# Kernel tuning notes

Measured on AMD Instinct MI355X. Metric: run time of the kernel, lower is better.

## Reference

```python
import jax, jax.numpy as jnp
import numpy as np

B, Q, K, D, H = 2, 1024, 4096, 1024, 16
DH = D // H
LN_EPS = 1e-5


def setup_inputs() -> dict:
    key = jax.random.key(0)
    ks = jax.random.split(key, 10)
    queries = jax.random.normal(ks[0], (B, Q, D), jnp.float32)
    keys = jax.random.normal(ks[1], (B, K, D), jnp.float32)
    values = jax.random.normal(ks[2], (B, K, D), jnp.float32)
    # 128 words of 8 query tokens each: boundaries 0,8,...,1024 (sorted, unique)
    word_boundaries = jnp.arange(0, Q + 1, 8, dtype=jnp.int32)  # [129]
    # monotone map from query positions to char/key positions in [0, K]
    char_boundaries = jnp.sort(jax.random.randint(ks[3], (Q,), 0, K + 1, dtype=jnp.int32))
    s = 0.02
    ln_gamma = jnp.ones((D,), jnp.float32)
    ln_beta = jnp.zeros((D,), jnp.float32)
    in_proj_w = jax.random.normal(ks[4], (3 * D, D), jnp.float32) * s
    in_proj_b = jnp.zeros((3 * D,), jnp.float32)
    out_w = jax.random.normal(ks[5], (D, D), jnp.float32) * s
    out_b = jnp.zeros((D,), jnp.float32)
    return dict(queries=queries, keys=keys, values=values,
                word_boundaries=word_boundaries, char_boundaries=char_boundaries,
                ln_gamma=ln_gamma, ln_beta=ln_beta,
                in_proj_w=in_proj_w, in_proj_b=in_proj_b,
                out_w=out_w, out_b=out_b)


def char_aware_mask(wb, cb, q_len, k_len):
    """Vectorized version of the per-word python loop.
    Float mask of 0/1 (PyTorch ADDS a float attn_mask to the scores)."""
    ws, we = wb[:-1], wb[1:]                     # word start/end in query coords [nW]
    nW = ws.shape[0]
    cs = cb[ws]                                  # char span start per word
    ce = cb[we - 1]                              # char span end per word
    q = jnp.arange(q_len)
    i = jnp.clip(jnp.searchsorted(wb, q, side='right') - 1, 0, nW - 1)  # word id per query row
    valid = (q >= ws[i]) & (q < we[i])           # rows actually written by the loop
    j = jnp.arange(k_len)[None, :]               # [1, K]
    in_char = (j >= cs[i][:, None]) & (j < ce[i][:, None])
    # prev word: keys [wb[i-1], wb[i]) (query-coord indices used on key axis, as in source)
    ps = ws[jnp.maximum(i - 1, 0)]
    in_prev = (i > 0)[:, None] & (j >= ps[:, None]) & (j < ws[i][:, None])
    # next word: keys [wb[i+1], wb[i+2])
    ns = we[i]
    ne = wb[jnp.minimum(i + 2, nW)]
    in_next = (i < nW - 1)[:, None] & (j >= ns[:, None]) & (j < ne[:, None])
    return (valid[:, None] & (in_char | in_prev | in_next)).astype(jnp.float32)


def reference(queries, keys, values, word_boundaries, char_boundaries,
              ln_gamma, ln_beta, in_proj_w, in_proj_b, out_w, out_b):
    b, q_len, d = queries.shape
    k_len = keys.shape[1]
    mask = char_aware_mask(word_boundaries, char_boundaries, q_len, k_len)  # [Q, K]
    # LayerNorm(queries)
    mu = jnp.mean(queries, axis=-1, keepdims=True)
    var = jnp.var(queries, axis=-1, keepdims=True)
    x = (queries - mu) * jax.lax.rsqrt(var + LN_EPS) * ln_gamma + ln_beta
    # MultiheadAttention(x, keys, values, attn_mask=mask) -- float mask added to logits
    wq, wk, wv = jnp.split(in_proj_w, 3, axis=0)
    bq, bk, bv = jnp.split(in_proj_b, 3)
    qh = (x @ wq.T + bq).reshape(b, q_len, H, DH)
    kh = (keys @ wk.T + bk).reshape(b, k_len, H, DH)
    vh = (values @ wv.T + bv).reshape(b, k_len, H, DH)
    scale = 1.0 / jnp.sqrt(jnp.asarray(DH, queries.dtype))
    scores = jnp.einsum('bqhd,bkhd->bhqk', qh * scale, kh) + mask[None, None]
    attn = jax.nn.softmax(scores, axis=-1)
    ctx = jnp.einsum('bhqk,bkhd->bqhd', attn, vh).reshape(b, q_len, d)
    out = ctx @ out_w.T + out_b
    # residual; dropout is identity at inference
    return queries + out
```

## Files before the change

### kernel.cpp

```cpp
#include <hip/hip_runtime.h>
#include <hip/hip_bf16.h>


typedef __attribute__((ext_vector_type(8))) short bf16x8;
typedef __attribute__((ext_vector_type(4))) float f32x4;
typedef __attribute__((ext_vector_type(16))) float f32x16;

#define L2E 1.44269504088896341f
#define CSCALE (0.125f * L2E)
#define NSPLIT 4

__device__ __forceinline__ short f2bf(float f) {
  __hip_bfloat16 h = __float2bfloat16(f);
  return reinterpret_cast<short&>(h);
}

__device__ __forceinline__ unsigned cvtpk(float a, float b) {
  unsigned r;
  asm("v_cvt_pk_bf16_f32 %0, %1, %2" : "=v"(r) : "v"(a), "v"(b));
  return r;
}

__device__ __forceinline__ float fexp2(float x) {
#if __has_builtin(__builtin_amdgcn_exp2f)
  return __builtin_amdgcn_exp2f(x);
#else
  float r;
  asm("v_exp_f32 %0, %1" : "=v"(r) : "v"(x));
  return r;
#endif
}

__device__ __forceinline__ void halfswap(unsigned a, unsigned b, unsigned& x, unsigned& y) {
#if __has_builtin(__builtin_amdgcn_permlane32_swap)
  auto r = __builtin_amdgcn_permlane32_swap(a, b, false, false);
  x = (unsigned)r[0];
  y = (unsigned)r[1];
#else
  unsigned ca = (unsigned)__shfl_xor((int)a, 32);
  unsigned cb = (unsigned)__shfl_xor((int)b, 32);
  bool h = ((threadIdx.x & 63) >> 5) != 0;
  x = h ? cb : a;
  y = h ? b : ca;
#endif
}

__device__ __forceinline__ void gload16(const void* g, void* l) {
  __builtin_amdgcn_global_load_lds(
      (const __attribute__((address_space(1))) void*)g,
      (__attribute__((address_space(3))) void*)l, 16, 0, 0);
}

template <int N>
__device__ __forceinline__ void pipe_barrier() {
  __builtin_amdgcn_sched_barrier(0);
  if constexpr (N == 8)
    asm volatile("s_waitcnt vmcnt(8) lgkmcnt(0)" ::: "memory");
  else if constexpr (N == 6)
    asm volatile("s_waitcnt vmcnt(6) lgkmcnt(0)" ::: "memory");
  else if constexpr (N == 2)
    asm volatile("s_waitcnt vmcnt(2) lgkmcnt(0)" ::: "memory");
  else
    asm volatile("s_waitcnt vmcnt(0) lgkmcnt(0)" ::: "memory");
  __builtin_amdgcn_s_barrier();
  __builtin_amdgcn_sched_barrier(0);
}

__device__ __forceinline__ void lds_barrier() {
  __builtin_amdgcn_sched_barrier(0);
  __builtin_amdgcn_s_barrier();
  __builtin_amdgcn_sched_barrier(0);
}

__global__ __launch_bounds__(256) void prep_kernel(const float* __restrict__ w,
                                                   const float* __restrict__ o,
                                                   short* __restrict__ dw,
                                                   short* __restrict__ dof,
                                                   const float* __restrict__ x,
                                                   const float* __restrict__ gamma,
                                                   const float* __restrict__ beta,
                                                   short* __restrict__ xout,
                                                   const int* __restrict__ wb,
                                                   const int* __restrict__ cb,
                                                   int* __restrict__ iv,
                                                   const float* __restrict__ keys,
                                                   const float* __restrict__ values,
                                                   short* __restrict__ kbf,
                                                   short* __restrict__ vbf) {
  const int blk = blockIdx.x;
  const int t = threadIdx.x;
  if (blk < 4096) {
    long i = ((long)blk * 256 + t) * 4;
    const float* s;
    short* d;
    if (i < 3145728) { s = w + i; d = dw + i; }
    else { s = o + (i - 3145728); d = dof + (i - 3145728); }
    float4 xv = *(const float4*)s;
    uint2 r;
    r.x = cvtpk(xv.x, xv.y);
    r.y = cvtpk(xv.z, xv.w);
    *(uint2*)d = r;
  } else if (blk < 6144) {
    const int row = blk - 4096;
    float4 v = ((const float4*)(x + (size_t)row * 1024))[t];
    float s = v.x + v.y + v.z + v.w;
    float ss = v.x * v.x + v.y * v.y + v.z * v.z + v.w * v.w;
#pragma unroll
    for (int d = 32; d; d >>= 1) { s += __shfl_xor(s, d); ss += __shfl_xor(ss, d); }
    __shared__ float red[8];
    int wv2 = t >> 6, lane = t & 63;
    if (lane == 0) { red[wv2] = s; red[4 + wv2] = ss; }
    __syncthreads();
    s = red[0] + red[1] + red[2] + red[3];
    ss = red[4] + red[5] + red[6] + red[7];
    float mean = s * (1.0f / 1024.0f);
    float var = ss * (1.0f / 1024.0f) - mean * mean;
    float rstd = rsqrtf(var + 1e-5f);
    float4 g = ((const float4*)gamma)[t];
    float4 b = ((const float4*)beta)[t];
    uint2 oo;
    oo.x = cvtpk((v.x - mean) * rstd * g.x + b.x, (v.y - mean) * rstd * g.y + b.y);
    oo.y = cvtpk((v.z - mean) * rstd * g.z + b.z, (v.w - mean) * rstd * g.w + b.w);
    ((uint2*)(xout + (size_t)row * 1024))[t] = oo;
  } else if (blk < 6148) {
    int q = (blk - 6144) * 256 + t;
    if (q >= 1024) return;
    int cnt = 0;
    for (int k = 0; k < 129; ++k) cnt += (wb[k] <= q) ? 1 : 0;
    int i = cnt - 1;
    i = i < 0 ? 0 : (i > 127 ? 127 : i);
    bool valid = (q >= wb[i]) && (q < wb[i + 1]);
    int cs = 0, ce = 0, pl = 0, ph = 0, nl = 0, nh = 0;
    if (valid) {
      cs = cb[wb[i]];
      ce = cb[wb[i + 1] - 1];
      if (i > 0) { pl = wb[i - 1]; ph = wb[i]; }
      if (i < 127) { nl = wb[i + 1]; nh = wb[(i + 2 <= 128) ? i + 2 : 128]; }
    }
    int* p = iv + q * 8;
    p[0] = cs; p[1] = ce; p[2] = pl; p[3] = ph; p[4] = nl; p[5] = nh; p[6] = 0; p[7] = 0;
  } else {
    long i = ((long)(blk - 6148) * 256 + t) * 4;
    const float* s;
    short* d;
    if (i < 8388608) { s = keys + i; d = kbf + i; }
    else { s = values + (i - 8388608); d = vbf + (i - 8388608); }
    float4 xv = *(const float4*)s;
    uint2 r;
    r.x = cvtpk(xv.x, xv.y);
    r.y = cvtpk(xv.z, xv.w);
    *(uint2*)d = r;
  }
}

__device__ __forceinline__ unsigned inrange3(int key, const int* p) {
  bool m = (key >= p[0] && key < p[1]) || (key >= p[2] && key < p[3]) ||
           (key >= p[4] && key < p[5]);
  return m ? 1u : 0u;
}

__global__ __launch_bounds__(256) void mask_frag_kernel(const int* __restrict__ iv,
                                                        uint4* __restrict__ pmf) {
  int idx = blockIdx.x * 256 + threadIdx.x;
  int lane = idx & 63;
  int wg = (idx >> 6) & 31;
  int t = idx >> 11;
  int l31 = lane & 31, hi = lane >> 5;
  uint4 o = {0u, 0u, 0u, 0u};
  if (!hi) {
    int key0 = t * 64 + l31, key1 = key0 + 32;
    const int* p0 = iv + (wg * 32 + 0) * 8;
    const int* p1 = iv + (wg * 32 + 8) * 8;
    const int* p2 = iv + (wg * 32 + 16) * 8;
    const int* p3 = iv + (wg * 32 + 24) * 8;
    unsigned b0 = inrange3(key0, p0), b1 = inrange3(key0, p1);
    unsigned b2 = inrange3(key0, p2), b3 = inrange3(key0, p3);
    o.x = (b0 | (b1 << 16)) * 0x3F80u;
    o.y = (b2 | (b3 << 16)) * 0x3F80u;
    b0 = inrange3(key1, p0); b1 = inrange3(key1, p1);
    b2 = inrange3(key1, p2); b3 = inrange3(key1, p3);
    o.z = (b0 | (b1 << 16)) * 0x3F80u;
    o.w = (b2 | (b3 << 16)) * 0x3F80u;
  }
  pmf[idx] = o;
}

__device__ __forceinline__ void kv256_body(short* lds, const short* __restrict__ Agl,
                                           const short* __restrict__ Bgl,
                                           const float* __restrict__ bias,
                                           short* __restrict__ Cout, int mode,
                                           int bx, int by) {
  const int tid = (int)threadIdx.x;
  const int lane = tid & 63;
  const int w = tid >> 6;
  const int wm = w >> 2, wn = w & 3;
  const int l16 = lane & 15, lhi = lane >> 4;
  const int gc8 = (lane & 7) ^ (lane >> 3);
  const int lr = lane >> 3;
  const int rsw = (l16 & 7) << 4;
  const int m0 = bx * 256, n0 = by * 256;

  f32x4 acc[8][4];
#pragma unroll
  for (int i = 0; i < 8; ++i)
#pragma unroll
    for (int j = 0; j < 4; ++j) acc[i][j] = f32x4{0.f, 0.f, 0.f, 0.f};

  auto STAGE = [&](int t, int bsel) {
    const int k0 = t * 64;
    short* dA = lds + bsel * 32768;
    short* dB = dA + 16384;
#pragma unroll
    for (int j = 0; j < 4; ++j) {
      int ch = w * 4 + j;
      gload16(Agl + (size_t)(m0 + ch * 8 + lr) * 1024 + k0 + gc8 * 8, dA + ch * 512);
      gload16(Bgl + (size_t)(n0 + ch * 8 + lr) * 1024 + k0 + gc8 * 8, dB + ch * 512);
    }
  };

  auto COMPUTE = [&](int bsel) {
    const char* cA = (const char*)(lds + bsel * 32768);
    const char* cB = cA + 32768;
#pragma unroll
    for (int kk = 0; kk < 2; ++kk) {
      bf16x8 af[8], bfr[4];
#pragma unroll
      for (int mt = 0; mt < 8; ++mt)
        af[mt] = *(const bf16x8*)(cA + (wm * 128 + mt * 16 + l16) * 128 +
                                  ((kk * 64 + lhi * 16) ^ rsw));
#pragma unroll
      for (int nt = 0; nt < 4; ++nt)
        bfr[nt] = *(const bf16x8*)(cB + (wn * 64 + nt * 16 + l16) * 128 +
                                   ((kk * 64 + lhi * 16) ^ rsw));
#pragma unroll
      for (int mt = 0; mt < 8; ++mt)
#pragma unroll
        for (int nt = 0; nt < 4; ++nt)
          acc[mt][nt] = __builtin_amdgcn_mfma_f32_16x16x32_bf16(af[mt], bfr[nt],
                                                                acc[mt][nt], 0, 0, 0);
    }
  };

  STAGE(0, 0);
  STAGE(1, 1);
  for (int t = 0; t < 15; ++t) {
    pipe_barrier<8>();
    COMPUTE(t & 1);
    lds_barrier();
    if (t < 14) STAGE(t + 2, t & 1);
  }
  pipe_barrier<0>();
  COMPUTE(1);

#pragma unroll
  for (int mt = 0; mt < 8; ++mt)
#pragma unroll
    for (int nt = 0; nt < 4; ++nt) {
      int n = n0 + wn * 64 + nt * 16 + l16;
#pragma unroll
      for (int r = 0; r < 4; ++r) {
        int m = m0 + wm * 128 + mt * 16 + lhi * 4 + r;
        float v = acc[mt][nt][r];
        if (mode == 0) {
          int bb = m >> 12, key = m & 4095;
          int hh = n >> 6, dhl = n & 63;
          Cout[((size_t)((bb * 16 + hh) * 4096 + key)) * 64 + dhl] = f2bf(v + bias[n]);
        } else {
          int bb = n >> 12, key = n & 4095;
          Cout[((size_t)(bb * 1024 + m)) * 4096 + key] = f2bf(v + bias[m]);
        }
      }
    }
}

__device__ __forceinline__ void gemmQO_body(short* lA, short* lB,
                                            const short* __restrict__ A,
                                            const short* __restrict__ W,
                                            const float* __restrict__ bias,
                                            const float* __restrict__ resid,
                                            void* __restrict__ Cout, int mode,
                                            float scale, int bxi, int byi) {
  const int lane = threadIdx.x & 63;
  const int w = threadIdx.x >> 6;
  const int m0 = bxi * 64;
  const int n0 = byi * 128;
  const int wm = w >> 2, wn = w & 3;
  const int l16 = lane & 15, lhi = lane >> 4;

  const int gc8 = (lane & 7) ^ (lane >> 3);
  const int lr = lane >> 3;
  const int rsw = (l16 & 7) << 4;

  f32x4 zero = {0.f, 0.f, 0.f, 0.f};
  f32x4 acc[2][2];
#pragma unroll
  for (int i = 0; i < 2; ++i)
#pragma unroll
    for (int j = 0; j < 2; ++j) acc[i][j] = zero;

  for (int k0 = 0; k0 < 1024; k0 += 64) {
    __syncthreads();
#pragma unroll
    for (int j = 0; j < 3; ++j) {
      int c = w * 3 + j;
      if (c < 8)
        gload16(A + (size_t)(m0 + c * 8 + lr) * 1024 + k0 + gc8 * 8, &lA[c * 512]);
      else
        gload16(W + (size_t)(n0 + (c - 8) * 8 + lr) * 1024 + k0 + gc8 * 8,
                &lB[(c - 8) * 512]);
    }
    __syncthreads();
    bf16x8 af[2][2], bfr[2][2];
#pragma unroll
    for (int mt = 0; mt < 2; ++mt)
#pragma unroll
      for (int kk = 0; kk < 2; ++kk)
        af[mt][kk] = *(const bf16x8*)((const char*)lA + (wm * 32 + mt * 16 + l16) * 128 +
                                      ((kk * 64 + lhi * 16) ^ rsw));
#pragma unroll
    for (int nt = 0; nt < 2; ++nt)
#pragma unroll
      for (int kk = 0; kk < 2; ++kk)
        bfr[nt][kk] = *(const bf16x8*)((const char*)lB + (wn * 32 + nt * 16 + l16) * 128 +
                                       ((kk * 64 + lhi * 16) ^ rsw));
#pragma unroll
    for (int kk = 0; kk < 2; ++kk)
#pragma unroll
      for (int mt = 0; mt < 2; ++mt)
#pragma unroll
        for (int nt = 0; nt < 2; ++nt)
          acc[mt][nt] = __builtin_amdgcn_mfma_f32_16x16x32_bf16(af[mt][kk], bfr[nt][kk],
                                                                acc[mt][nt], 0, 0, 0);
  }

#pragma unroll
  for (int mt = 0; mt < 2; ++mt)
#pragma unroll
    for (int nt = 0; nt < 2; ++nt) {
      int col = n0 + wn * 32 + nt * 16 + l16;
      float bs = bias[col];
#pragma unroll
      for (int r = 0; r < 4; ++r) {
        int row = m0 + wm * 32 + mt * 16 + lhi * 4 + r;
        float v = acc[mt][nt][r] + bs;
        if (mode == 0) {
          ((short*)Cout)[(size_t)row * 1024 + col] = f2bf(v * scale);
        } else {
          size_t idx = (size_t)row * 1024 + col;
          ((float*)Cout)[idx] = v + resid[idx];
        }
      }
    }
}

__global__ __launch_bounds__(512, 2) void megaGemm_kernel(const short* __restrict__ kbf,
                                                          const short* __restrict__ wk,
                                                          const float* __restrict__ kbias,
                                                          const short* __restrict__ wv,
                                                          const short* __restrict__ vbf,
                                                          const float* __restrict__ vbias,
                                                          short* __restrict__ khp,
                                                          short* __restrict__ vhT,
                                                          const short* __restrict__ xb,
                                                          const short* __restrict__ wq,
                                                          const float* __restrict__ qbias,
                                                          short* __restrict__ qhb) {
  __shared__ __attribute__((aligned(16))) short lds[65536];
  int id = blockIdx.x;
  if (id < 128) {
    kv256_body(lds, kbf, wk, kbias, khp, 0, id & 31, id >> 5);
  } else if (id < 256) {
    int i2 = id & 127;
    kv256_body(lds, wv, vbf, vbias, vhT, 1, i2 >> 5, i2 & 31);
  } else {
    int i2 = id - 256;
    gemmQO_body(lds, lds + 4096, xb, wq, qbias, nullptr, qhb, 0, CSCALE, i2 & 31, i2 >> 5);
  }
}

__global__ __launch_bounds__(512, 4) void gemmQO_kernel(const short* __restrict__ A,
                                                        const short* __restrict__ W,
                                                        const float* __restrict__ bias,
                                                        const float* __restrict__ resid,
                                                        void* __restrict__ Cout, int mode,
                                                        float scale) {
  __shared__ __attribute__((aligned(16))) short lA[4096];
  __shared__ __attribute__((aligned(16))) short lB[8192];
  gemmQO_body(lA, lB, A, W, bias, resid, Cout, mode, scale, blockIdx.x, blockIdx.y);
}

__global__ __launch_bounds__(256) void attn9_kernel(const short* __restrict__ qh,
                                                    const short* __restrict__ khp,
                                                    const short* __restrict__ vtp,
                                                    const uint4* __restrict__ pmf,
                                                    short* __restrict__ pacc,
                                                    float* __restrict__ pml) {
  const int tid = threadIdx.x;
  const int lane = tid & 63;
  const int w = tid >> 6;
  const int l31 = lane & 31;
  const int hi = lane >> 5;
  const int id = blockIdx.x;
  const int qb = id >> 7;
  const int g = id & 127;
  const int bh = g >> 2;
  const int ks = g & 3;
  const int b = bh >> 4, h = bh & 15;

  __shared__ __attribute__((aligned(16))) short sK[2][4096];
  __shared__ __attribute__((aligned(16))) short sV[2][4096];

  const int wq0 = qb * 128 + w * 32;
  const int qrow = wq0 + l31;
  bf16x8 qf0, qf1, qf2, qf3;
  {
    const short* qp = qh + ((size_t)(b * 1024 + qrow)) * 1024 + h * 64 + hi * 8;
    qf0 = *(const bf16x8*)(qp);
    qf1 = *(const bf16x8*)(qp + 16);
    qf2 = *(const bf16x8*)(qp + 32);
    qf3 = *(const bf16x8*)(qp + 48);
  }

  bf16x8 bmv;
  {
    union { unsigned u[4]; bf16x8 v; } t;
    t.u[0] = t.u[1] = t.u[2] = t.u[3] = 0;
    int lj = l31 >> 3;
    unsigned val = 0x3FB9u << (16 * (lj & 1));
    if (!hi) t.u[lj >> 1] = val;
    bmv = t.v;
  }

  bf16x8 bones;
  {
    union { unsigned u[4]; bf16x8 v; } t;
    t.u[0] = t.u[1] = t.u[2] = t.u[3] = 0x3F803F80u;
    bones = t.v;
  }

  f32x16 fzero;
#pragma unroll
  for (int i = 0; i < 16; ++i) fzero[i] = 0.f;

  const int kchunk = ks * 1024;
  const int sub = (lane & 7) ^ (lane >> 3);
  const int r8 = lane >> 3;
  const size_t kbase_g = ((size_t)bh * 4096 + kchunk) * 64;
  const size_t vbase_g = ((size_t)bh * 64) * 4096 + (size_t)kchunk;
  const uint4* pmfp = pmf + ((size_t)(ks * 16) * 32 + qb * 4 + w) * 64 + lane;

  f32x16 acc0, acc1, acc2;
#pragma unroll
  for (int i = 0; i < 16; ++i) { acc0[i] = 0.f; acc1[i] = 0.f; acc2[i] = 0.f; }

  const int koff_swz = (lane & 7) << 4;

  auto STAGE = [&](int buf, int t) {
    int kt = t * 64;
#pragma unroll
    for (int q2 = 0; q2 < 2; ++q2) {
      int ch = w * 2 + q2;
      gload16(khp + kbase_g + (size_t)(kt + ch * 8 + r8) * 64 + sub * 8,
              (short*)sK[buf] + ch * 512);
      gload16(vtp + vbase_g + (size_t)(ch * 8 + r8) * 4096 + kt + sub * 8,
              (short*)sV[buf] + ch * 512);
    }
  };

  uint4 mf_cur = pmfp[0];
  uint4 mf_next = mf_cur;
  STAGE(0, 0);
  __syncthreads();
  int buf = 0;

  for (int t = 0; t < 16; ++t) {
    if (t < 15) {
      STAGE(buf ^ 1, t + 1);
      mf_next = pmfp[(size_t)(t + 1) * 2048];
    }

    bf16x8 am0, am1;
    {
      union { unsigned u[4]; bf16x8 v; } f;
      f.u[0] = mf_cur.x; f.u[1] = mf_cur.y; f.u[2] = 0; f.u[3] = 0;
      am0 = f.v;
      f.u[0] = mf_cur.z; f.u[1] = mf_cur.w;
      am1 = f.v;
    }

    __builtin_amdgcn_s_setprio(1);
    f32x16 ss0 = __builtin_amdgcn_mfma_f32_32x32x16_bf16(am0, bmv, fzero, 0, 0, 0);
    f32x16 ss1 = __builtin_amdgcn_mfma_f32_32x32x16_bf16(am1, bmv, fzero, 0, 0, 0);
#pragma unroll
    for (int c = 0; c < 4; ++c) {
      int off = (c * 32 + hi * 16) ^ koff_swz;
      bf16x8 k0 = *(const bf16x8*)((const char*)sK[buf] + l31 * 128 + off);
      bf16x8 k1 = *(const bf16x8*)((const char*)sK[buf] + (32 + l31) * 128 + off);
      bf16x8 qc = (c == 0) ? qf0 : (c == 1) ? qf1 : (c == 2) ? qf2 : qf3;
      ss0 = __builtin_amdgcn_mfma_f32_32x32x16_bf16(k0, qc, ss0, 0, 0, 0);
      ss1 = __builtin_amdgcn_mfma_f32_32x32x16_bf16(k1, qc, ss1, 0, 0, 0);
    }
    __builtin_amdgcn_s_setprio(0);

#pragma unroll
    for (int r = 0; r < 16; ++r) {
      ss0[r] = fexp2(ss0[r]);
      ss1[r] = fexp2(ss1[r]);
    }

    bf16x8 pa0, pa1, pa2, pa3;
    {
      unsigned a01 = cvtpk(ss0[0], ss0[1]), a23 = cvtpk(ss0[2], ss0[3]);
      unsigned a45 = cvtpk(ss0[4], ss0[5]), a67 = cvtpk(ss0[6], ss0[7]);
      unsigned a89 = cvtpk(ss0[8], ss0[9]), aAB = cvtpk(ss0[10], ss0[11]);
      unsigned aCD = cvtpk(ss0[12], ss0[13]), aEF = cvtpk(ss0[14], ss0[15]);
      union { unsigned u[4]; bf16x8 v; } f;
      halfswap(a01, a45, f.u[0], f.u[2]);
      halfswap(a23, a67, f.u[1], f.u[3]);
      pa0 = f.v;
      halfswap(a89, aCD, f.u[0], f.u[2]);
      halfswap(aAB, aEF, f.u[1], f.u[3]);
      pa1 = f.v;
    }
    {
      unsigned a01 = cvtpk(ss1[0], ss1[1]), a23 = cvtpk(ss1[2], ss1[3]);
      unsigned a45 = cvtpk(ss1[4], ss1[5]), a67 = cvtpk(ss1[6], ss1[7]);
      unsigned a89 = cvtpk(ss1[8], ss1[9]), aAB = cvtpk(ss1[10], ss1[11]);
      unsigned aCD = cvtpk(ss1[12], ss1[13]), aEF = cvtpk(ss1[14], ss1[15]);
      union { unsigned u[4]; bf16x8 v; } f;
      halfswap(a01, a45, f.u[0], f.u[2]);
      halfswap(a23, a67, f.u[1], f.u[3]);
      pa2 = f.v;
      halfswap(a89, aCD, f.u[0], f.u[2]);
      halfswap(aAB, aEF, f.u[1], f.u[3]);
      pa3 = f.v;
    }

    __builtin_amdgcn_s_setprio(1);
#pragma unroll
    for (int kb16 = 0; kb16 < 4; ++kb16) {
      int off = (kb16 * 32 + hi * 16) ^ koff_swz;
      bf16x8 v0 = *(const bf16x8*)((const char*)sV[buf] + l31 * 128 + off);
      bf16x8 v1 = *(const bf16x8*)((const char*)sV[buf] + (32 + l31) * 128 + off);
      bf16x8 pa = (kb16 == 0) ? pa0 : (kb16 == 1) ? pa1 : (kb16 == 2) ? pa2 : pa3;
      acc0 = __builtin_amdgcn_mfma_f32_32x32x16_bf16(pa, v0, acc0, 0, 0, 0);
      acc1 = __builtin_amdgcn_mfma_f32_32x32x16_bf16(pa, v1, acc1, 0, 0, 0);
      acc2 = __builtin_amdgcn_mfma_f32_32x32x16_bf16(pa, bones, acc2, 0, 0, 0);
    }
    __builtin_amdgcn_s_setprio(0);
    __syncthreads();
    buf ^= 1;
    mf_cur = mf_next;
  }

  short* paccp = pacc + (((size_t)ks * 32 + bh) * 1024) * 64;
#pragma unroll
  for (int r = 0; r < 16; r += 2) {
    int q0 = wq0 + ((r & 3) + 8 * (r >> 2)) + 4 * hi;
    int q1 = wq0 + (((r + 1) & 3) + 8 * ((r + 1) >> 2)) + 4 * hi;
    unsigned u0 = cvtpk(acc0[r], acc0[r + 1]);
    unsigned u1 = cvtpk(acc1[r], acc1[r + 1]);
    paccp[(size_t)q0 * 64 + l31] = (short)(u0 & 0xffffu);
    paccp[(size_t)q1 * 64 + l31] = (short)(u0 >> 16);
    paccp[(size_t)q0 * 64 + 32 + l31] = (short)(u1 & 0xffffu);
    paccp[(size_t)q1 * 64 + 32 + l31] = (short)(u1 >> 16);
  }
  if (l31 == 0) {
    float* mlp = pml + ((size_t)ks * 32 + bh) * 1024;
#pragma unroll
    for (int r = 0; r < 16; ++r) {
      int q = wq0 + ((r & 3) + 8 * (r >> 2)) + 4 * hi;
      mlp[q] = acc2[r];
    }
  }
}

__global__ __launch_bounds__(256) void combine_kernel(const short* __restrict__ pacc,
                                                      const float* __restrict__ pml,
                                                      short* __restrict__ ctx) {
  int idx = blockIdx.x * 256 + threadIdx.x;
  int dh4 = idx & 15;
  int row = idx >> 4;
  int bh = row >> 10, q = row & 1023;
  float L = 0.f, o0 = 0.f, o1 = 0.f, o2 = 0.f, o3 = 0.f;
#pragma unroll
  for (int k = 0; k < NSPLIT; ++k) {
    L += pml[((size_t)k * 32 + bh) * 1024 + q];
    uint2 u = *(const uint2*)&pacc[(((size_t)k * 32 + bh) * 1024 + q) * 64 + dh4 * 4];
    unsigned a = u.x, b2 = u.y;
    unsigned t0 = a << 16, t1 = a & 0xffff0000u, t2 = b2 << 16, t3 = b2 & 0xffff0000u;
    o0 += reinterpret_cast<float&>(t0);
    o1 += reinterpret_cast<float&>(t1);
    o2 += reinterpret_cast<float&>(t2);
    o3 += reinterpret_cast<float&>(t3);
  }
  float inv = 1.0f / L;
  uint2 st;
  st.x = cvtpk(o0 * inv, o1 * inv);
  st.y = cvtpk(o2 * inv, o3 * inv);
  int b = bh >> 4, h = bh & 15;
  *(uint2*)&ctx[((size_t)(b * 1024 + q)) * 1024 + h * 64 + dh4 * 4] = st;
}

extern "C" void kernel_launch(void* const* d_in, const int* in_sizes, int n_in,
                              void* d_out, int out_size, void* d_ws, size_t ws_size,
                              hipStream_t stream) {
  const float* queries = (const float*)d_in[0];
  const float* keys    = (const float*)d_in[1];
  const float* values  = (const float*)d_in[2];
  const int*   wb      = (const int*)d_in[3];
  const int*   cb      = (const int*)d_in[4];
  const float* gamma   = (const float*)d_in[5];
  const float* beta    = (const float*)d_in[6];
  const float* ipw     = (const float*)d_in[7];
  const float* ipb     = (const float*)d_in[8];
  const float* ow      = (const float*)d_in[9];
  const float* ob      = (const float*)d_in[10];
  float* out = (float*)d_out;

  char* p = (char*)d_ws;
  short* xb  = (short*)p; p += (size_t)2048 * 1024 * 2;
  short* kb  = (short*)p; p += (size_t)8192 * 1024 * 2;
  short* vb  = (short*)p; p += (size_t)8192 * 1024 * 2;
  short* wpb = (short*)p; p += (size_t)3072 * 1024 * 2;
  short* owb = (short*)p; p += (size_t)1024 * 1024 * 2;
  short* qhb = (short*)p; p += (size_t)2048 * 1024 * 2;
  short* khp = (short*)p; p += (size_t)8192 * 1024 * 2;
  short* vhT = (short*)p; p += (size_t)8192 * 1024 * 2;
  short* ctx = (short*)p; p += (size_t)2048 * 1024 * 2;
  int* iv = (int*)p; p += (size_t)1024 * 8 * 4;
  uint4* pmf = (uint4*)p; p += (size_t)64 * 32 * 64 * 16;
  if ((size_t)(p - (char*)d_ws) > ws_size) return;

  short* pacc = kb;
  float* pml  = (float*)wpb;

  prep_kernel<<<22532, 256, 0, stream>>>(ipw, ow, wpb, owb, queries, gamma, beta, xb,
                                         wb, cb, iv, keys, values, kb, vb);
  mask_frag_kernel<<<512, 256, 0, stream>>>(iv, pmf);

  megaGemm_kernel<<<512, 512, 0, stream>>>(kb, wpb + 1048576, ipb + 1024,
                                           wpb + 2097152, vb, ipb + 2048,
                                           khp, vhT, xb, wpb, ipb, qhb);

  attn9_kernel<<<1024, 256, 0, stream>>>(qhb, khp, vhT, pmf, pacc, pml);
  combine_kernel<<<2048, 256, 0, stream>>>(pacc, pml, ctx);

  gemmQO_kernel<<<dim3(32, 8), 512, 0, stream>>>(ctx, owb, ob, queries, out, 2, 1.f);
}
```

Measured before the change: 151.4 us.

## Interleave GEMM K-tile loads with quadrant MFMA phases in projection kernel

Restructures the 256x256 bf16 GEMM main loop. Each K-tile is now split into four quadrant compute phases, and the global-to-LDS loads for upcoming tiles are issued in sub-units between them, with a finer waitcnt/barrier schedule instead of one load-all and compute-all step per tile. MFMA blocks run at raised wave priority via s_setprio. The aim is to overlap memory loads with matrix math and to lower register pressure from fragments. The risks are more barriers per tile and subtle LDS hazards in the hand-written schedule.

Result: no change. 154.2 us (+1.8%).

```diff
diff --git a/kernel.cpp b/kernel.cpp
--- a/kernel.cpp
+++ b/kernel.cpp
@@ -52,23 +52,25 @@
 }
 
 template <int N>
-__device__ __forceinline__ void pipe_barrier() {
+__device__ __forceinline__ void phase_end() {
   __builtin_amdgcn_sched_barrier(0);
   if constexpr (N == 8)
-    asm volatile("s_waitcnt vmcnt(8) lgkmcnt(0)" ::: "memory");
+    asm volatile("s_waitcnt vmcnt(8)" ::: "memory");
   else if constexpr (N == 6)
-    asm volatile("s_waitcnt vmcnt(6) lgkmcnt(0)" ::: "memory");
+    asm volatile("s_waitcnt vmcnt(6)" ::: "memory");
+  else if constexpr (N == 4)
+    asm volatile("s_waitcnt vmcnt(4)" ::: "memory");
   else if constexpr (N == 2)
-    asm volatile("s_waitcnt vmcnt(2) lgkmcnt(0)" ::: "memory");
+    asm volatile("s_waitcnt vmcnt(2)" ::: "memory");
   else
-    asm volatile("s_waitcnt vmcnt(0) lgkmcnt(0)" ::: "memory");
+    asm volatile("s_waitcnt vmcnt(0)" ::: "memory");
   __builtin_amdgcn_s_barrier();
   __builtin_amdgcn_sched_barrier(0);
 }
 
-__device__ __forceinline__ void lds_barrier() {
+__device__ __forceinline__ void wait_lgkm0() {
   __builtin_amdgcn_sched_barrier(0);
-  __builtin_amdgcn_s_barrier();
+  asm volatile("s_waitcnt lgkmcnt(0)" ::: "memory");
   __builtin_amdgcn_sched_barrier(0);
 }
 
@@ -206,51 +208,92 @@
 #pragma unroll
     for (int j = 0; j < 4; ++j) acc[i][j] = f32x4{0.f, 0.f, 0.f, 0.f};
 
-  auto STAGE = [&](int t, int bsel) {
-    const int k0 = t * 64;
-    short* dA = lds + bsel * 32768;
-    short* dB = dA + 16384;
-#pragma unroll
-    for (int j = 0; j < 4; ++j) {
-      int ch = w * 4 + j;
-      gload16(Agl + (size_t)(m0 + ch * 8 + lr) * 1024 + k0 + gc8 * 8, dA + ch * 512);
-      gload16(Bgl + (size_t)(n0 + ch * 8 + lr) * 1024 + k0 + gc8 * 8, dB + ch * 512);
+  auto SU = [&](int k, int unit) {
+    const int k0 = k * 64;
+    short* base = lds + (k & 1) * 32768;
+#pragma unroll
+    for (int j = 0; j < 2; ++j) {
+      int i = w * 2 + j;
+      int ch;
+      bool isA;
+      if (unit == 1)      { ch = (i < 8) ? i : i + 8;       isA = true; }
+      else if (unit == 4) { ch = 8 + ((i < 8) ? i : i + 8); isA = true; }
+      else if (unit == 2) { ch = (i >> 2) * 8 + (i & 3);    isA = false; }
+      else                { ch = 4 + (i >> 2) * 8 + (i & 3); isA = false; }
+      const short* g = isA ? (Agl + (size_t)(m0 + ch * 8 + lr) * 1024 + k0 + gc8 * 8)
+                           : (Bgl + (size_t)(n0 + ch * 8 + lr) * 1024 + k0 + gc8 * 8);
+      gload16(g, base + (isA ? 0 : 16384) + ch * 512);
     }
   };
 
-  auto COMPUTE = [&](int bsel) {
+  bf16x8 af[4][2], b0[2][2], b1[2][2];
+  auto LDA = [&](int bsel, int qm) {
     const char* cA = (const char*)(lds + bsel * 32768);
-    const char* cB = cA + 32768;
-#pragma unroll
-    for (int kk = 0; kk < 2; ++kk) {
-      bf16x8 af[8], bfr[4];
-#pragma unroll
-      for (int mt = 0; mt < 8; ++mt)
-        af[mt] = *(const bf16x8*)(cA + (wm * 128 + mt * 16 + l16) * 128 +
-                                  ((kk * 64 + lhi * 16) ^ rsw));
-#pragma unroll
-      for (int nt = 0; nt < 4; ++nt)
-        bfr[nt] = *(const bf16x8*)(cB + (wn * 64 + nt * 16 + l16) * 128 +
-                                   ((kk * 64 + lhi * 16) ^ rsw));
-#pragma unroll
-      for (int mt = 0; mt < 8; ++mt)
-#pragma unroll
-        for (int nt = 0; nt < 4; ++nt)
-          acc[mt][nt] = __builtin_amdgcn_mfma_f32_16x16x32_bf16(af[mt], bfr[nt],
-                                                                acc[mt][nt], 0, 0, 0);
-    }
+#pragma unroll
+    for (int mt = 0; mt < 4; ++mt)
+#pragma unroll
+      for (int kk = 0; kk < 2; ++kk) {
+        int row = wm * 128 + qm * 64 + mt * 16 + l16;
+        af[mt][kk] = *(const bf16x8*)(cA + row * 128 + ((kk * 64 + lhi * 16) ^ rsw));
+      }
   };
-
-  STAGE(0, 0);
-  STAGE(1, 1);
-  for (int t = 0; t < 15; ++t) {
-    pipe_barrier<8>();
-    COMPUTE(t & 1);
-    lds_barrier();
-    if (t < 14) STAGE(t + 2, t & 1);
-  }
-  pipe_barrier<0>();
-  COMPUTE(1);
+  auto LDB = [&](int bsel, int qn, bf16x8 (&bf)[2][2]) {
+    const char* cB = (const char*)(lds + bsel * 32768) + 32768;
+#pragma unroll
+    for (int nt = 0; nt < 2; ++nt)
+#pragma unroll
+      for (int kk = 0; kk < 2; ++kk) {
+        int row = wn * 64 + qn * 32 + nt * 16 + l16;
+        bf[nt][kk] = *(const bf16x8*)(cB + row * 128 + ((kk * 64 + lhi * 16) ^ rsw));
+      }
+  };
+  auto MM = [&](int qm, int qn, bf16x8 (&bf)[2][2]) {
+    __builtin_amdgcn_s_setprio(1);
+#pragma unroll
+    for (int kk = 0; kk < 2; ++kk)
+#pragma unroll
+      for (int mt = 0; mt < 4; ++mt)
+#pragma unroll
+        for (int nt = 0; nt < 2; ++nt)
+          acc[qm * 4 + mt][qn * 2 + nt] = __builtin_amdgcn_mfma_f32_16x16x32_bf16(
+              af[mt][kk], bf[nt][kk], acc[qm * 4 + mt][qn * 2 + nt], 0, 0, 0);
+    __builtin_amdgcn_s_setprio(0);
+  };
+
+  SU(0, 1); SU(0, 2); SU(0, 3); SU(0, 4);
+  SU(1, 1); SU(1, 2);
+  phase_end<8>();
+
+#pragma unroll 2
+  for (int k = 0; k < 14; ++k) {
+    const int bs = k & 1;
+    LDA(bs, 0); LDB(bs, 0, b0); SU(k + 1, 3);
+    wait_lgkm0(); MM(0, 0, b0); phase_end<8>();
+    LDB(bs, 1, b1); SU(k + 1, 4);
+    wait_lgkm0(); MM(0, 1, b1); phase_end<8>();
+    LDA(bs, 1); SU(k + 2, 1);
+    wait_lgkm0(); MM(1, 0, b0); phase_end<8>();
+    SU(k + 2, 2);
+    MM(1, 1, b1); phase_end<8>();
+  }
+  {
+    LDA(0, 0); LDB(0, 0, b0); SU(15, 3);
+    wait_lgkm0(); MM(0, 0, b0); phase_end<8>();
+    LDB(0, 1, b1); SU(15, 4);
+    wait_lgkm0(); MM(0, 1, b1); phase_end<8>();
+    LDA(0, 1);
+    wait_lgkm0(); MM(1, 0, b0); phase_end<8>();
+    MM(1, 1, b1); phase_end<4>();
+  }
+  {
+    LDA(1, 0); LDB(1, 0, b0);
+    wait_lgkm0(); MM(0, 0, b0); phase_end<2>();
+    LDB(1, 1, b1);
+    wait_lgkm0(); MM(0, 1, b1); phase_end<0>();
+    LDA(1, 1);
+    wait_lgkm0(); MM(1, 0, b0);
+    MM(1, 1, b1);
+  }
 
 #pragma unroll
   for (int mt = 0; mt < 8; ++mt)
```
